# Performance work log

Measured on AMD Instinct MI355X. Metric: run time of the kernel, lower is better.

Reference implementation:

```python
import jax, jax.numpy as jnp
import numpy as np

B, S, D_IN, D_OUT, HID, E, SHARE, TOPK = 4, 2048, 1024, 1024, 2048, 8, 1, 2


def setup_inputs() -> dict:
    key = jax.random.key(0)
    ks = jax.random.split(key, 12)
    s_in = 1.0 / np.sqrt(D_IN)
    s_hid = 1.0 / np.sqrt(HID)
    return {
        "x": jax.random.normal(ks[0], (B, S, D_IN), jnp.float32),
        "gate_w": jax.random.normal(ks[1], (D_IN, E), jnp.float32) * s_in,
        "gate_b": jnp.zeros((E,), jnp.float32),
        "ew1": jax.random.normal(ks[2], (E, D_IN, HID), jnp.float32) * s_in,
        "eb1": jnp.zeros((E, HID), jnp.float32),
        "ew2": jax.random.normal(ks[3], (E, HID, D_OUT), jnp.float32) * s_hid,
        "eb2": jnp.zeros((E, D_OUT), jnp.float32),
        "sw1": jax.random.normal(ks[4], (SHARE, D_IN, HID), jnp.float32) * s_in,
        "sb1": jnp.zeros((SHARE, HID), jnp.float32),
        "sw2": jax.random.normal(ks[5], (SHARE, HID, D_OUT), jnp.float32) * s_hid,
        "sb2": jnp.zeros((SHARE, D_OUT), jnp.float32),
        "top_k": TOPK,
    }


def reference(x, gate_w, gate_b, ew1, eb1, ew2, eb2, sw1, sb1, sw2, sb2, top_k):
    Bx, Sx, Din = x.shape
    flat_x = x.reshape(-1, Din)                      # [T, D]
    T = flat_x.shape[0]
    Ex = gate_w.shape[1]

    # gate + softmax + top-k, renormalize top-k weights
    logits = flat_x @ gate_w + gate_b                # [T, E]
    expert_weights = jax.nn.softmax(logits, axis=-1)
    topv, topi = jax.lax.top_k(expert_weights, top_k)
    topv = topv / jnp.sum(topv, axis=-1, keepdims=True)

    # per-token combine weights scattered into [T, E] (zero for unselected)
    combine = jnp.zeros((T, Ex), flat_x.dtype)
    combine = combine.at[jnp.arange(T)[:, None], topi].add(topv)

    # expert MLPs (BasicExpert: Linear -> ReLU -> Linear), batched over experts
    h = jax.nn.relu(jnp.einsum("td,edh->teh", flat_x, ew1) + eb1)   # [T, E, H]
    eo = jnp.einsum("teh,eho->teo", h, ew2) + eb2                    # [T, E, O]
    moe_out = jnp.einsum("teo,te->to", eo, combine)                  # [T, O]
    final = moe_out.reshape(Bx, Sx, -1)

    # shared experts added densely to every token
    for k in range(sw1.shape[0]):
        sh = jax.nn.relu(jnp.einsum("bsd,dh->bsh", x, sw1[k]) + sb1[k])
        final = final + jnp.einsum("bsh,ho->bso", sh, sw2[k]) + sb2[k]

    return final, expert_weights
```

## Files before the change

kernel.cpp:

```cpp
#include <hip/hip_runtime.h>
#include <hip/hip_bf16.h>
#include <stdint.h>

#define T_TOK 8192
#define DIN   1024
#define DOUT  1024
#define HID   2048
#define NEXP  8
#define MAXN  8192

typedef __attribute__((ext_vector_type(8))) short short8;
typedef __attribute__((ext_vector_type(4))) float floatx4;

__device__ __forceinline__ ushort f2bf(float f) {
    uint32_t u = __float_as_uint(f);
    uint32_t r = (u + 0x7fffu + ((u >> 16) & 1u)) >> 16;
    return (ushort)r;
}

__device__ __forceinline__ void load_lds_16(const ushort* g, ushort* l) {
    __builtin_amdgcn_global_load_lds(
        (const __attribute__((address_space(1))) void*)g,
        (__attribute__((address_space(3))) void*)l, 16, 0, 0);
}

__global__ void convert_x_kernel(const float* __restrict__ in, ushort* __restrict__ out, int n4) {
    int i = blockIdx.x * blockDim.x + threadIdx.x;
    if (i >= n4) return;
    float4 v = ((const float4*)in)[i];
    ushort4 o;
    o.x = f2bf(v.x); o.y = f2bf(v.y); o.z = f2bf(v.z); o.w = f2bf(v.w);
    ((ushort4*)out)[i] = o;
}

__global__ void transpose_bf16_kernel(const float* __restrict__ in, ushort* __restrict__ out,
                                      int R, int C) {
    __shared__ float tile[64][65];
    size_t base = (size_t)blockIdx.z * R * C;
    in  += base;
    out += base;
    int r0 = blockIdx.y * 64, c0 = blockIdx.x * 64;
    int t  = threadIdx.x;
    int rr = t >> 4;
    int cc = (t & 15) * 4;
    for (int p = 0; p < 4; p++) {
        int row = rr + p * 16;
        float4 v = *(const float4*)(in + (size_t)(r0 + row) * C + c0 + cc);
        tile[row][cc + 0] = v.x; tile[row][cc + 1] = v.y;
        tile[row][cc + 2] = v.z; tile[row][cc + 3] = v.w;
    }
    __syncthreads();
    for (int p = 0; p < 4; p++) {
        int orow = rr + p * 16;
        ushort4 o;
        o.x = f2bf(tile[cc + 0][orow]);
        o.y = f2bf(tile[cc + 1][orow]);
        o.z = f2bf(tile[cc + 2][orow]);
        o.w = f2bf(tile[cc + 3][orow]);
        *(ushort4*)(out + (size_t)(c0 + orow) * R + r0 + cc) = o;
    }
}

__global__ void gate_compute_kernel(const float* __restrict__ x, const float* __restrict__ gw,
                                    const float* __restrict__ gb, float* __restrict__ ew_out,
                                    int* __restrict__ te1, int* __restrict__ te2,
                                    float* __restrict__ tw1, float* __restrict__ tw2) {
    int gid  = blockIdx.x * blockDim.x + threadIdx.x;
    int t    = gid >> 6;
    int lane = threadIdx.x & 63;
    if (t >= T_TOK) return;
    float acc[8];
    #pragma unroll
    for (int e = 0; e < 8; e++) acc[e] = 0.f;
    const float* xrow = x + (size_t)t * DIN;
    #pragma unroll
    for (int i = 0; i < 16; i++) {
        int d = lane + i * 64;
        float xv = xrow[d];
        const float4* wr = (const float4*)(gw + (size_t)d * 8);
        float4 w0 = wr[0], w1 = wr[1];
        acc[0] += xv * w0.x; acc[1] += xv * w0.y; acc[2] += xv * w0.z; acc[3] += xv * w0.w;
        acc[4] += xv * w1.x; acc[5] += xv * w1.y; acc[6] += xv * w1.z; acc[7] += xv * w1.w;
    }
    #pragma unroll
    for (int e = 0; e < 8; e++)
        #pragma unroll
        for (int off = 32; off; off >>= 1) acc[e] += __shfl_xor(acc[e], off);
    if (lane == 0) {
        float l[8], mx = -1e30f;
        #pragma unroll
        for (int e = 0; e < 8; e++) { l[e] = acc[e] + gb[e]; mx = fmaxf(mx, l[e]); }
        float s = 0.f;
        #pragma unroll
        for (int e = 0; e < 8; e++) { l[e] = expf(l[e] - mx); s += l[e]; }
        float inv = 1.f / s;
        #pragma unroll
        for (int e = 0; e < 8; e++) { l[e] *= inv; ew_out[(size_t)t * 8 + e] = l[e]; }
        int i1 = 0;
        #pragma unroll
        for (int e = 1; e < 8; e++) if (l[e] > l[i1]) i1 = e;
        int i2 = (i1 == 0) ? 1 : 0;
        #pragma unroll
        for (int e = 0; e < 8; e++) if (e != i1 && l[e] > l[i2]) i2 = e;
        float s2 = l[i1] + l[i2];
        te1[t] = i1; tw1[t] = l[i1] / s2;
        te2[t] = i2; tw2[t] = l[i2] / s2;
    }
}

__global__ void build_lists_kernel(const int* __restrict__ te1, const int* __restrict__ te2,
                                   const float* __restrict__ tw1, const float* __restrict__ tw2,
                                   int* __restrict__ counts, int* __restrict__ etok,
                                   float* __restrict__ ew) {
    __shared__ int lcnt[NEXP];
    __shared__ int gbase[NEXP];
    int tid = threadIdx.x;
    int t = blockIdx.x * 256 + tid;
    if (tid < NEXP) lcnt[tid] = 0;
    __syncthreads();
    int e1 = te1[t], e2 = te2[t];
    float w1 = tw1[t], w2 = tw2[t];
    int r1 = atomicAdd(&lcnt[e1], 1);
    int r2 = atomicAdd(&lcnt[e2], 1);
    __syncthreads();
    if (tid < NEXP) gbase[tid] = atomicAdd(&counts[tid], lcnt[tid]);
    __syncthreads();
    int s1 = gbase[e1] + r1;
    etok[e1 * MAXN + s1] = t;
    ew  [e1 * MAXN + s1] = w1;
    int s2 = gbase[e2] + r2;
    etok[e2 * MAXN + s2] = t;
    ew  [e2 * MAXN + s2] = w2;
}

__global__ void prefix_kernel(const int* __restrict__ counts, int* __restrict__ offsets) {
    if (threadIdx.x == 0 && blockIdx.x == 0) {
        int o = 0;
        for (int e = 0; e < NEXP; e++) { offsets[e] = o; o += counts[e]; }
    }
}

template <int MODE>
__global__ __launch_bounds__(256)
void gemm_kernel(const ushort* __restrict__ A, const ushort* __restrict__ Bt,
                 const float* __restrict__ bias, ushort* __restrict__ Hout,
                 float* __restrict__ Out,
                 const int* __restrict__ counts, const int* __restrict__ offsets,
                 const int* __restrict__ expert_tok, const float* __restrict__ expert_w,
                 int K) {
    const int e = blockIdx.z;
    int cnt, rowbase = 0;
    size_t bt_off = 0;
    const float* bcol = bias;
    if constexpr (MODE == 0) {
        cnt = counts[e]; rowbase = offsets[e];
        bt_off = (size_t)e * HID * DIN; bcol = bias + (size_t)e * HID;
    } else if constexpr (MODE == 1) {
        cnt = T_TOK;
    } else if constexpr (MODE == 2) {
        cnt = counts[e]; rowbase = offsets[e];
        bt_off = (size_t)e * DOUT * HID; bcol = bias + (size_t)e * DOUT;
    } else {
        cnt = T_TOK;
    }

    const int m0 = blockIdx.y * 128;
    if (m0 >= cnt) return;
    const int n0 = blockIdx.x * 128;

    __shared__ ushort As[8192];
    __shared__ ushort Bs[8192];
    __shared__ int    rowA[128];
    __shared__ int    rowTok[128];
    __shared__ float  rowW[128];

    const int tid = threadIdx.x;
    if (tid < 128) {
        int g = m0 + tid;
        if constexpr (MODE == 0) {
            rowA[tid] = (g < cnt) ? expert_tok[e * MAXN + g] : 0;
        } else if constexpr (MODE == 1) {
            rowA[tid] = g;
        } else if constexpr (MODE == 2) {
            rowA[tid]   = (g < cnt) ? (rowbase + g) : rowbase;
            rowTok[tid] = (g < cnt) ? expert_tok[e * MAXN + g] : 0;
            rowW[tid]   = (g < cnt) ? expert_w[e * MAXN + g] : 0.f;
        } else {
            rowA[tid] = g;
        }
    }
    __syncthreads();

    const int wave = tid >> 6, lane = tid & 63;
    const int lm = lane & 15, lq = lane >> 4;

    const ushort* gA[4];
    const ushort* gB[4];
    ushort* dA[4];
    ushort* dB[4];
    #pragma unroll
    for (int i = 0; i < 4; i++) {
        int b = wave * 4 + i;
        int rblk = b >> 1, kkb = b & 1;
        int r = rblk * 16 + lm;
        gA[i] = A + (size_t)rowA[r] * K + kkb * 32 + lq * 8;
        gB[i] = Bt + bt_off + (size_t)(n0 + r) * K + kkb * 32 + lq * 8;
        dA[i] = &As[b * 512];
        dB[i] = &Bs[b * 512];
    }

    floatx4 acc[4][4];
    #pragma unroll
    for (int i = 0; i < 4; i++)
        #pragma unroll
        for (int j = 0; j < 4; j++) acc[i][j] = (floatx4){0.f, 0.f, 0.f, 0.f};

    for (int k0 = 0; k0 < K; k0 += 64) {
        #pragma unroll
        for (int i = 0; i < 4; i++) {
            load_lds_16(gA[i] + k0, dA[i]);
            load_lds_16(gB[i] + k0, dB[i]);
        }
        __syncthreads();
        #pragma unroll
        for (int kkb = 0; kkb < 2; kkb++) {
            short8 afr[4], bfr[4];
            #pragma unroll
            for (int mt = 0; mt < 4; mt++)
                afr[mt] = *(const short8*)&As[(((wave >> 1) * 4 + mt) * 2 + kkb) * 512 + lane * 8];
            #pragma unroll
            for (int nt = 0; nt < 4; nt++)
                bfr[nt] = *(const short8*)&Bs[(((wave & 1) * 4 + nt) * 2 + kkb) * 512 + lane * 8];
            #pragma unroll
            for (int mt = 0; mt < 4; mt++)
                #pragma unroll
                for (int nt = 0; nt < 4; nt++)
                    acc[mt][nt] = __builtin_amdgcn_mfma_f32_16x16x32_bf16(
                        afr[mt], bfr[nt], acc[mt][nt], 0, 0, 0);
        }
        __syncthreads();
    }

    const int wm = (wave >> 1) * 64, wn = (wave & 1) * 64;
    #pragma unroll
    for (int mt = 0; mt < 4; mt++) {
        int rl_base = wm + mt * 16 + lq * 4;
        #pragma unroll
        for (int nt = 0; nt < 4; nt++) {
            int col = n0 + wn + nt * 16 + lm;
            float bv = bcol[col];
            #pragma unroll
            for (int r = 0; r < 4; r++) {
                int rl = rl_base + r;
                int g  = m0 + rl;
                float v = acc[mt][nt][r];
                if constexpr (MODE == 0) {
                    if (g < cnt) {
                        v = fmaxf(v + bv, 0.f);
                        Hout[(size_t)(rowbase + g) * HID + col] = f2bf(v);
                    }
                } else if constexpr (MODE == 1) {
                    v = fmaxf(v + bv, 0.f);
                    Hout[(size_t)g * HID + col] = f2bf(v);
                } else if constexpr (MODE == 2) {
                    if (g < cnt) {
                        v = (v + bv) * rowW[rl];
                        atomicAdd(&Out[(size_t)rowTok[rl] * DOUT + col], v);
                    }
                } else {
                    atomicAdd(&Out[(size_t)g * DOUT + col], v + bv);
                }
            }
        }
    }
}

extern "C" void kernel_launch(void* const* d_in, const int* in_sizes, int n_in,
                              void* d_out, int out_size, void* d_ws, size_t ws_size,
                              hipStream_t stream) {
    const float* x   = (const float*)d_in[0];
    const float* gw  = (const float*)d_in[1];
    const float* gb  = (const float*)d_in[2];
    const float* ew1 = (const float*)d_in[3];
    const float* eb1 = (const float*)d_in[4];
    const float* ew2 = (const float*)d_in[5];
    const float* eb2 = (const float*)d_in[6];
    const float* sw1 = (const float*)d_in[7];
    const float* sb1 = (const float*)d_in[8];
    const float* sw2 = (const float*)d_in[9];
    const float* sb2 = (const float*)d_in[10];

    float* out_final = (float*)d_out;
    float* out_ew    = out_final + (size_t)T_TOK * DOUT;

    char* ws = (char*)d_ws;
    size_t off = 0;
    auto alloc = [&](size_t bytes) -> void* {
        void* p = ws + off;
        off += (bytes + 255) & ~(size_t)255;
        return p;
    };
    ushort* x_bf    = (ushort*)alloc((size_t)T_TOK * DIN * 2);
    ushort* ew1t    = (ushort*)alloc((size_t)NEXP * HID * DIN * 2);
    ushort* ew2t    = (ushort*)alloc((size_t)NEXP * DOUT * HID * 2);
    ushort* sw1t    = (ushort*)alloc((size_t)HID * DIN * 2);
    ushort* sw2t    = (ushort*)alloc((size_t)DOUT * HID * 2);
    ushort* h_buf   = (ushort*)alloc((size_t)T_TOK * 2 * HID * 2);
    ushort* sh_buf  = (ushort*)alloc((size_t)T_TOK * HID * 2);
    int*    counts  = (int*)alloc(NEXP * 4);
    int*    offsets = (int*)alloc(NEXP * 4);
    int*    etok    = (int*)alloc((size_t)NEXP * MAXN * 4);
    float*  ew      = (float*)alloc((size_t)NEXP * MAXN * 4);
    int*    te1     = (int*)alloc((size_t)T_TOK * 4);
    int*    te2     = (int*)alloc((size_t)T_TOK * 4);
    float*  tw1     = (float*)alloc((size_t)T_TOK * 4);
    float*  tw2     = (float*)alloc((size_t)T_TOK * 4);

    hipMemsetAsync(d_out, 0, (size_t)T_TOK * DOUT * 4, stream);
    hipMemsetAsync(counts, 0, NEXP * 4, stream);

    convert_x_kernel<<<(T_TOK * DIN / 4) / 256, 256, 0, stream>>>(x, x_bf, T_TOK * DIN / 4);
    transpose_bf16_kernel<<<dim3(HID / 64, DIN / 64, NEXP), 256, 0, stream>>>(ew1, ew1t, DIN, HID);
    transpose_bf16_kernel<<<dim3(DOUT / 64, HID / 64, NEXP), 256, 0, stream>>>(ew2, ew2t, HID, DOUT);
    transpose_bf16_kernel<<<dim3(HID / 64, DIN / 64, 1), 256, 0, stream>>>(sw1, sw1t, DIN, HID);
    transpose_bf16_kernel<<<dim3(DOUT / 64, HID / 64, 1), 256, 0, stream>>>(sw2, sw2t, HID, DOUT);

    gate_compute_kernel<<<T_TOK / 4, 256, 0, stream>>>(x, gw, gb, out_ew, te1, te2, tw1, tw2);
    build_lists_kernel<<<T_TOK / 256, 256, 0, stream>>>(te1, te2, tw1, tw2, counts, etok, ew);
    prefix_kernel<<<1, 64, 0, stream>>>(counts, offsets);

    gemm_kernel<0><<<dim3(HID / 128, MAXN / 128, NEXP), 256, 0, stream>>>(
        x_bf, ew1t, eb1, h_buf, nullptr, counts, offsets, etok, ew, DIN);
    gemm_kernel<1><<<dim3(HID / 128, T_TOK / 128, 1), 256, 0, stream>>>(
        x_bf, sw1t, sb1, sh_buf, nullptr, counts, offsets, etok, ew, DIN);
    gemm_kernel<2><<<dim3(DOUT / 128, MAXN / 128, NEXP), 256, 0, stream>>>(
        h_buf, ew2t, eb2, nullptr, out_final, counts, offsets, etok, ew, HID);
    gemm_kernel<3><<<dim3(DOUT / 128, T_TOK / 128, 1), 256, 0, stream>>>(
        sh_buf, sw2t, sb2, nullptr, out_final, counts, offsets, etok, ew, HID);
}
```

Baseline: 799.0 us.

## Use 256x256 multi-stage pipelined MFMA GEMM and merge expert and shared launches

```diff
diff --git a/kernel.cpp b/kernel.cpp
--- a/kernel.cpp
+++ b/kernel.cpp
@@ -1,5 +1,4 @@
 #include <hip/hip_runtime.h>
-#include <hip/hip_bf16.h>
 #include <stdint.h>
 
 #define T_TOK 8192
@@ -140,135 +139,179 @@
     }
 }
 
+
+#define STG(slot, j, kh) { \
+    load_lds_16(srcA[j] + (size_t)(kh) * 32, dA[j] + (slot) * 8192); \
+    load_lds_16(srcB[j] + (size_t)(kh) * 32, dB[j] + (slot) * 8192); }
+
+#define LDA_FRAGS(slot, mh) { \
+    const ushort* pa = &lA[(slot) * 8192 + (wave_m * 8 + (mh) * 4) * 512 + lane * 8]; \
+    a[0] = *(const short8*)(pa +    0); a[1] = *(const short8*)(pa +  512); \
+    a[2] = *(const short8*)(pa + 1024); a[3] = *(const short8*)(pa + 1536); }
+
+#define LDB_FRAGS(slot) { \
+    const ushort* pb = &lB[(slot) * 8192 + (wave_n * 4) * 512 + lane * 8]; \
+    b[0] = *(const short8*)(pb +    0); b[1] = *(const short8*)(pb +  512); \
+    b[2] = *(const short8*)(pb + 1024); b[3] = *(const short8*)(pb + 1536); }
+
+#define MFMA16(mh) { \
+    _Pragma("unroll") for (int mt = 0; mt < 4; ++mt) { \
+      _Pragma("unroll") for (int nt = 0; nt < 4; ++nt) { \
+        acc[(mh)*4+mt][nt] = __builtin_amdgcn_mfma_f32_16x16x32_bf16( \
+            a[mt], b[nt], acc[(mh)*4+mt][nt], 0, 0, 0); } } }
+
+#define PH_EVEN(slot, sslot, kh) { \
+    LDA_FRAGS(slot, 0); LDB_FRAGS(slot); \
+    STG(sslot, 0, kh); \
+    __builtin_amdgcn_s_barrier(); \
+    asm volatile("s_waitcnt lgkmcnt(0)" ::: "memory"); \
+    __builtin_amdgcn_sched_barrier(0); \
+    __builtin_amdgcn_s_setprio(1); \
+    MFMA16(0); \
+    __builtin_amdgcn_s_setprio(0); \
+    __builtin_amdgcn_s_barrier(); \
+    asm volatile("" ::: "memory"); }
+
+#define PH_ODD(slot, sslot, kh) { \
+    LDA_FRAGS(slot, 1); \
+    STG(sslot, 1, kh); \
+    __builtin_amdgcn_s_barrier(); \
+    asm volatile("s_waitcnt lgkmcnt(0)" ::: "memory"); \
+    __builtin_amdgcn_sched_barrier(0); \
+    __builtin_amdgcn_s_setprio(1); \
+    MFMA16(1); \
+    __builtin_amdgcn_s_setprio(0); \
+    asm volatile("s_waitcnt vmcnt(8)" ::: "memory"); \
+    __builtin_amdgcn_s_barrier(); \
+    asm volatile("" ::: "memory"); }
+
 template <int MODE>
-__global__ __launch_bounds__(256)
-void gemm_kernel(const ushort* __restrict__ A, const ushort* __restrict__ Bt,
-                 const float* __restrict__ bias, ushort* __restrict__ Hout,
-                 float* __restrict__ Out,
-                 const int* __restrict__ counts, const int* __restrict__ offsets,
-                 const int* __restrict__ expert_tok, const float* __restrict__ expert_w,
-                 int K) {
-    const int e = blockIdx.z;
-    int cnt, rowbase = 0;
-    size_t bt_off = 0;
-    const float* bcol = bias;
-    if constexpr (MODE == 0) {
-        cnt = counts[e]; rowbase = offsets[e];
-        bt_off = (size_t)e * HID * DIN; bcol = bias + (size_t)e * HID;
-    } else if constexpr (MODE == 1) {
-        cnt = T_TOK;
-    } else if constexpr (MODE == 2) {
-        cnt = counts[e]; rowbase = offsets[e];
-        bt_off = (size_t)e * DOUT * HID; bcol = bias + (size_t)e * DOUT;
+__global__ __launch_bounds__(512, 2)
+void gemm8_kernel(const ushort* __restrict__ Ae, const ushort* __restrict__ Ash,
+                  const ushort* __restrict__ Be, const ushort* __restrict__ Bsh,
+                  const float* __restrict__ biase, const float* __restrict__ biass,
+                  ushort* __restrict__ He, ushort* __restrict__ Hs,
+                  float* __restrict__ Out,
+                  const int* __restrict__ counts, const int* __restrict__ offsets,
+                  const int* __restrict__ expert_tok, const float* __restrict__ expert_w) {
+    constexpr int K  = (MODE == 0) ? DIN : HID;
+    constexpr int NN = (MODE == 0) ? HID : DOUT;
+    constexpr int NH = K / 32;
+    constexpr int J  = K / 128;
+
+    const int z  = blockIdx.z;
+    const int m0 = blockIdx.y * 256;
+    const int n0 = blockIdx.x * 256;
+
+    int cnt = T_TOK, rowbase = 0;
+    const ushort* Aptr; const ushort* Bptr; const float* bptr;
+    if (z < NEXP) {
+        cnt = counts[z];
+        if (m0 >= cnt) return;
+        rowbase = offsets[z];
+        Aptr = Ae; Bptr = Be + (size_t)z * NN * K; bptr = biase + (size_t)z * NN;
     } else {
-        cnt = T_TOK;
-    }
-
-    const int m0 = blockIdx.y * 128;
-    if (m0 >= cnt) return;
-    const int n0 = blockIdx.x * 128;
-
-    __shared__ ushort As[8192];
-    __shared__ ushort Bs[8192];
-    __shared__ int    rowA[128];
-    __shared__ int    rowTok[128];
-    __shared__ float  rowW[128];
+        Aptr = Ash; Bptr = Bsh; bptr = biass;
+    }
+
+    __shared__ ushort lA[4 * 8192];
+    __shared__ ushort lB[4 * 8192];
+    __shared__ int    rowA[256];
+    __shared__ int    rowTok[256];
+    __shared__ float  rowW[256];
 
     const int tid = threadIdx.x;
-    if (tid < 128) {
+    if (tid < 256) {
         int g = m0 + tid;
-        if constexpr (MODE == 0) {
-            rowA[tid] = (g < cnt) ? expert_tok[e * MAXN + g] : 0;
-        } else if constexpr (MODE == 1) {
-            rowA[tid] = g;
-        } else if constexpr (MODE == 2) {
-            rowA[tid]   = (g < cnt) ? (rowbase + g) : rowbase;
-            rowTok[tid] = (g < cnt) ? expert_tok[e * MAXN + g] : 0;
-            rowW[tid]   = (g < cnt) ? expert_w[e * MAXN + g] : 0.f;
+        if (z < NEXP) {
+            if constexpr (MODE == 0) {
+                rowA[tid] = (g < cnt) ? expert_tok[z * MAXN + g] : 0;
+            } else {
+                rowA[tid]   = (g < cnt) ? (rowbase + g) : rowbase;
+                rowTok[tid] = (g < cnt) ? expert_tok[z * MAXN + g] : 0;
+                rowW[tid]   = (g < cnt) ? expert_w[z * MAXN + g] : 0.f;
+            }
         } else {
             rowA[tid] = g;
         }
     }
     __syncthreads();
 
-    const int wave = tid >> 6, lane = tid & 63;
+    const int w = tid >> 6, lane = tid & 63;
     const int lm = lane & 15, lq = lane >> 4;
-
-    const ushort* gA[4];
-    const ushort* gB[4];
-    ushort* dA[4];
-    ushort* dB[4];
-    #pragma unroll
-    for (int i = 0; i < 4; i++) {
-        int b = wave * 4 + i;
-        int rblk = b >> 1, kkb = b & 1;
-        int r = rblk * 16 + lm;
-        gA[i] = A + (size_t)rowA[r] * K + kkb * 32 + lq * 8;
-        gB[i] = Bt + bt_off + (size_t)(n0 + r) * K + kkb * 32 + lq * 8;
-        dA[i] = &As[b * 512];
-        dB[i] = &Bs[b * 512];
-    }
-
-    floatx4 acc[4][4];
-    #pragma unroll
-    for (int i = 0; i < 4; i++)
-        #pragma unroll
-        for (int j = 0; j < 4; j++) acc[i][j] = (floatx4){0.f, 0.f, 0.f, 0.f};
-
-    for (int k0 = 0; k0 < K; k0 += 64) {
-        #pragma unroll
-        for (int i = 0; i < 4; i++) {
-            load_lds_16(gA[i] + k0, dA[i]);
-            load_lds_16(gB[i] + k0, dB[i]);
-        }
-        __syncthreads();
-        #pragma unroll
-        for (int kkb = 0; kkb < 2; kkb++) {
-            short8 afr[4], bfr[4];
+    const int wave_m = w >> 2, wave_n = w & 3;
+
+    const ushort* srcA[2]; const ushort* srcB[2];
+    ushort* dA[2]; ushort* dB[2];
+    #pragma unroll
+    for (int j = 0; j < 2; ++j) {
+        int blk = j * 8 + w;
+        srcA[j] = Aptr + (size_t)rowA[blk * 16 + lm] * K + lq * 8;
+        srcB[j] = Bptr + (size_t)(n0 + blk * 16 + lm) * K + lq * 8;
+        dA[j] = &lA[blk * 512];
+        dB[j] = &lB[blk * 512];
+    }
+
+    floatx4 acc[8][4];
+    #pragma unroll
+    for (int i = 0; i < 8; ++i)
+        #pragma unroll
+        for (int jj = 0; jj < 4; ++jj) acc[i][jj] = (floatx4){0.f, 0.f, 0.f, 0.f};
+
+    short8 a[4], b[4];
+
+    STG(0, 0, 0); STG(0, 1, 0);
+    STG(1, 0, 1); STG(1, 1, 1);
+    STG(2, 0, 2); STG(2, 1, 2);
+    asm volatile("s_waitcnt vmcnt(8)" ::: "memory");
+    __builtin_amdgcn_s_barrier();
+    asm volatile("" ::: "memory");
+
+    for (int j = 0; j < J; ++j) {
+        int k4 = 4 * j;
+        int kh3 = k4 + 3; if (kh3 > NH - 1) kh3 = NH - 1;
+        int kh4 = k4 + 4; if (kh4 > NH - 1) kh4 = NH - 1;
+        int kh5 = k4 + 5; if (kh5 > NH - 1) kh5 = NH - 1;
+        int kh6 = k4 + 6; if (kh6 > NH - 1) kh6 = NH - 1;
+        PH_EVEN(0, 3, kh3);
+        PH_ODD (0, 3, kh3);
+        PH_EVEN(1, 0, kh4);
+        PH_ODD (1, 0, kh4);
+        PH_EVEN(2, 1, kh5);
+        PH_ODD (2, 1, kh5);
+        PH_EVEN(3, 2, kh6);
+        PH_ODD (3, 2, kh6);
+    }
+
+    asm volatile("s_waitcnt vmcnt(0)" ::: "memory");
+
+    const int wn0 = wave_n * 64;
+    #pragma unroll
+    for (int mt8 = 0; mt8 < 8; ++mt8) {
+        const int rl0 = wave_m * 128 + mt8 * 16 + lq * 4;
+        #pragma unroll
+        for (int nt = 0; nt < 4; ++nt) {
+            const int col = n0 + wn0 + nt * 16 + lm;
+            const float bv = bptr[col];
             #pragma unroll
-            for (int mt = 0; mt < 4; mt++)
-                afr[mt] = *(const short8*)&As[(((wave >> 1) * 4 + mt) * 2 + kkb) * 512 + lane * 8];
-            #pragma unroll
-            for (int nt = 0; nt < 4; nt++)
-                bfr[nt] = *(const short8*)&Bs[(((wave & 1) * 4 + nt) * 2 + kkb) * 512 + lane * 8];
-            #pragma unroll
-            for (int mt = 0; mt < 4; mt++)
-                #pragma unroll
-                for (int nt = 0; nt < 4; nt++)
-                    acc[mt][nt] = __builtin_amdgcn_mfma_f32_16x16x32_bf16(
-                        afr[mt], bfr[nt], acc[mt][nt], 0, 0, 0);
-        }
-        __syncthreads();
-    }
-
-    const int wm = (wave >> 1) * 64, wn = (wave & 1) * 64;
-    #pragma unroll
-    for (int mt = 0; mt < 4; mt++) {
-        int rl_base = wm + mt * 16 + lq * 4;
-        #pragma unroll
-        for (int nt = 0; nt < 4; nt++) {
-            int col = n0 + wn + nt * 16 + lm;
-            float bv = bcol[col];
-            #pragma unroll
-            for (int r = 0; r < 4; r++) {
-                int rl = rl_base + r;
-                int g  = m0 + rl;
-                float v = acc[mt][nt][r];
+            for (int r = 0; r < 4; ++r) {
+                const int rl = rl0 + r;
+                const int g  = m0 + rl;
+                float v = acc[mt8][nt][r];
                 if constexpr (MODE == 0) {
-                    if (g < cnt) {
-                        v = fmaxf(v + bv, 0.f);
-                        Hout[(size_t)(rowbase + g) * HID + col] = f2bf(v);
-                    }
-                } else if constexpr (MODE == 1) {
                     v = fmaxf(v + bv, 0.f);
-                    Hout[(size_t)g * HID + col] = f2bf(v);
-                } else if constexpr (MODE == 2) {
-                    if (g < cnt) {
-                        v = (v + bv) * rowW[rl];
-                        atomicAdd(&Out[(size_t)rowTok[rl] * DOUT + col], v);
+                    if (z < NEXP) {
+                        if (g < cnt) He[(size_t)(rowbase + g) * HID + col] = f2bf(v);
+                    } else {
+                        Hs[(size_t)g * HID + col] = f2bf(v);
                     }
                 } else {
-                    atomicAdd(&Out[(size_t)g * DOUT + col], v + bv);
+                    if (z < NEXP) {
+                        if (g < cnt)
+                            atomicAdd(&Out[(size_t)rowTok[rl] * DOUT + col], (v + bv) * rowW[rl]);
+                    } else {
+                        atomicAdd(&Out[(size_t)g * DOUT + col], v + bv);
+                    }
                 }
             }
         }
@@ -329,12 +372,10 @@
     build_lists_kernel<<<T_TOK / 256, 256, 0, stream>>>(te1, te2, tw1, tw2, counts, etok, ew);
     prefix_kernel<<<1, 64, 0, stream>>>(counts, offsets);
 
-    gemm_kernel<0><<<dim3(HID / 128, MAXN / 128, NEXP), 256, 0, stream>>>(
-        x_bf, ew1t, eb1, h_buf, nullptr, counts, offsets, etok, ew, DIN);
-    gemm_kernel<1><<<dim3(HID / 128, T_TOK / 128, 1), 256, 0, stream>>>(
-        x_bf, sw1t, sb1, sh_buf, nullptr, counts, offsets, etok, ew, DIN);
-    gemm_kernel<2><<<dim3(DOUT / 128, MAXN / 128, NEXP), 256, 0, stream>>>(
-        h_buf, ew2t, eb2, nullptr, out_final, counts, offsets, etok, ew, HID);
-    gemm_kernel<3><<<dim3(DOUT / 128, T_TOK / 128, 1), 256, 0, stream>>>(
-        sh_buf, sw2t, sb2, nullptr, out_final, counts, offsets, etok, ew, HID);
-}
+    gemm8_kernel<0><<<dim3(HID / 256, T_TOK / 256, NEXP + 1), 512, 0, stream>>>(
+        x_bf, x_bf, ew1t, sw1t, eb1, sb1, h_buf, sh_buf, nullptr,
+        counts, offsets, etok, ew);
+    gemm8_kernel<1><<<dim3(DOUT / 256, T_TOK / 256, NEXP + 1), 512, 0, stream>>>(
+        h_buf, sh_buf, ew2t, sw2t, eb2, sb2, nullptr, nullptr, out_final,
+        counts, offsets, etok, ew);
+}
```

After: 694.9 us. 13.0% less time.
